# Performance work log

Hardware: AMD Instinct MI355X
Metric: run time of the kernel (lower is better)

Reference implementation:

```python
import jax, jax.numpy as jnp
import numpy as np

BN_EPS = 1e-5

def _batchnorm(z, gamma, beta):
    # training-mode BN over node axis, biased variance (matches torch normalization)
    mean = jnp.mean(z, axis=0)
    var = jnp.mean((z - mean) ** 2, axis=0)
    return (z - mean) * jax.lax.rsqrt(var + BN_EPS) * gamma + beta

def setup_inputs() -> dict:
    key = jax.random.key(0)
    N, E, D, L = 100000, 1000000, 128, 2
    ks = jax.random.split(key, 8)
    x = jax.random.normal(ks[0], (N, D), dtype=jnp.float32)
    edge_index = jax.random.randint(ks[1], (2, E), 0, N, dtype=jnp.int64)
    s = 1.0 / np.sqrt(D)
    W1 = jax.random.uniform(ks[2], (L, D, D), jnp.float32, -s, s)
    b1 = jax.random.uniform(ks[3], (L, D), jnp.float32, -s, s)
    W2 = jax.random.uniform(ks[4], (L, D, D), jnp.float32, -s, s)
    b2 = jax.random.uniform(ks[5], (L, D), jnp.float32, -s, s)
    g1 = jnp.ones((L, D), jnp.float32); bt1 = jnp.zeros((L, D), jnp.float32)
    g_out = jnp.ones((L, D), jnp.float32); bt_out = jnp.zeros((L, D), jnp.float32)
    eps = jnp.zeros((L,), jnp.float32)  # GIN eps, init 0
    return {"x": x, "edge_index": edge_index, "W1": W1, "b1": b1, "g1": g1,
            "bt1": bt1, "W2": W2, "b2": b2, "eps": eps, "g_out": g_out, "bt_out": bt_out}

def reference(x, edge_index, W1, b1, g1, bt1, W2, b2, eps, g_out, bt_out):
    N = x.shape[0]
    L = W1.shape[0]
    src, dst = edge_index[0], edge_index[1]
    h = x
    for l in range(L):
        # message: relu(x_j) gathered along edges; aggregate: scatter-add to dst
        msg = jax.nn.relu(h[src])                                  # [E, D]
        aggr = jax.ops.segment_sum(msg, dst, num_segments=N)       # [N, D]
        z = (1.0 + eps[l]) * h + aggr
        # GINConv MLP: Linear -> BN -> ReLU -> Linear
        z = z @ W1[l].T + b1[l]
        z = jax.nn.relu(_batchnorm(z, g1[l], bt1[l]))
        z = z @ W2[l].T + b2[l]
        # outer per-layer BatchNorm
        z = _batchnorm(z, g_out[l], bt_out[l])
        if l < L - 1:
            z = jax.nn.relu(z)
        # dropout is identity in eval mode
        h = z
    return h
```

## Files before the change

### kernel.cpp

```cpp
#include <hip/hip_runtime.h>
#include <hip/hip_fp16.h>

typedef unsigned int u32;
typedef unsigned short u16;
typedef __attribute__((ext_vector_type(8))) _Float16 f16x8;
typedef __attribute__((ext_vector_type(4))) float f32x4;

#define DF 128
#define NBUCK 256
#define BUCK_SHIFT 9
#define BUCK_SIZE 512
#define P2_CHUNK 4096
#define NCOPY 16
#define STATW (NCOPY * DF)
#define CS16 136

__device__ __forceinline__ __half2 u2h2(u32 x) { union { u32 u; __half2 h; } v; v.u = x; return v.h; }
__device__ __forceinline__ u32 h22u(__half2 h) { union { u32 u; __half2 h; } v; v.h = h; return v.u; }
__device__ __forceinline__ u32 pack2h(float a, float b) { return h22u(__floats2half2_rn(a, b)); }

__device__ __forceinline__ u32 pkmax_u(u32 a, u32 b) {
  u32 r;
  asm("v_pk_max_f16 %0, %1, %2" : "=v"(r) : "v"(a), "v"(b));
  return r;
}
__device__ __forceinline__ __half2 hmax2(__half2 a, __half2 b) {
  return u2h2(pkmax_u(h22u(a), h22u(b)));
}

__global__ void k_cvt_f32_f16(const float* __restrict__ in, u16* __restrict__ out, int n4) {
  int i = blockIdx.x * blockDim.x + threadIdx.x;
  if (i >= n4) return;
  float4 v = ((const float4*)in)[i];
  ((uint2*)out)[i] = make_uint2(pack2h(v.x, v.y), pack2h(v.z, v.w));
}

__global__ __launch_bounds__(256) void k_p1(const int* __restrict__ dst,
                                            int* __restrict__ bucketCount, int E) {
  __shared__ int h[NBUCK];
  int t = threadIdx.x;
  h[t] = 0;
  __syncthreads();
  for (int e = blockIdx.x * 256 + t; e < E; e += gridDim.x * 256)
    atomicAdd(&h[((u32)dst[e]) >> BUCK_SHIFT], 1);
  __syncthreads();
  if (h[t]) atomicAdd(&bucketCount[t], h[t]);
}

__global__ __launch_bounds__(256) void k_pscan(const int* __restrict__ bucketCount,
                                               int* __restrict__ bucketStart,
                                               int* __restrict__ bucketCursor,
                                               int* __restrict__ rowptr, int N, int E) {
  __shared__ int sh[NBUCK];
  int t = threadIdx.x;
  int c = bucketCount[t];
  sh[t] = c;
  __syncthreads();
  for (int o = 1; o < 256; o <<= 1) {
    int v = (t >= o) ? sh[t - o] : 0;
    __syncthreads();
    sh[t] += v;
    __syncthreads();
  }
  int excl = sh[t] - c;
  bucketStart[t] = excl;
  bucketCursor[t] = excl;
  if (t == 255) { bucketStart[256] = sh[255]; rowptr[N] = E; }
}

__global__ __launch_bounds__(256) void k_p2(const int* __restrict__ src,
                                            const int* __restrict__ dst,
                                            int* __restrict__ bucketCursor,
                                            uint2* __restrict__ part, int E) {
  __shared__ int h[NBUCK], hs[NBUCK], base[NBUCK];
  __shared__ int total;
  __shared__ uint2 buf[P2_CHUNK];
  int t = threadIdx.x;
  int e0 = blockIdx.x * P2_CHUNK;
  h[t] = 0;
  __syncthreads();
  int myb[16], myr[16];
  uint2 mye[16];
  #pragma unroll
  for (int k = 0; k < 16; k++) {
    int e = e0 + k * 256 + t;
    myb[k] = -1;
    if (e < E) {
      int s = src[e], d = dst[e];
      mye[k] = make_uint2((u32)s, (u32)d);
      myb[k] = ((u32)d) >> BUCK_SHIFT;
      myr[k] = atomicAdd(&h[myb[k]], 1);
    }
  }
  __syncthreads();
  int hc = h[t];
  hs[t] = hc;
  __syncthreads();
  for (int o = 1; o < 256; o <<= 1) {
    int v = (t >= o) ? hs[t - o] : 0;
    __syncthreads();
    hs[t] += v;
    __syncthreads();
  }
  if (t == 255) total = hs[255];
  int excl = hs[t] - hc;
  base[t] = hc ? atomicAdd(&bucketCursor[t], hc) : 0;
  __syncthreads();
  hs[t] = excl;
  __syncthreads();
  #pragma unroll
  for (int k = 0; k < 16; k++)
    if (myb[k] >= 0) buf[hs[myb[k]] + myr[k]] = mye[k];
  __syncthreads();
  int tot = total;
  for (int i = t; i < tot; i += 256) {
    uint2 ed = buf[i];
    int b = ed.y >> BUCK_SHIFT;
    part[base[b] + (i - hs[b])] = ed;
  }
}

__global__ __launch_bounds__(256) void k_p3(const uint2* __restrict__ part,
                                            const int* __restrict__ bucketStart,
                                            int* __restrict__ rowptr,
                                            int* __restrict__ adj, int N) {
  __shared__ int deg[BUCK_SIZE], cur[BUCK_SIZE], psum[256];
  int b = blockIdx.x, t = threadIdx.x;
  int nodeBase = b << BUCK_SHIFT;
  int eb = bucketStart[b], ee = bucketStart[b + 1];
  deg[t] = 0; deg[t + 256] = 0;
  __syncthreads();
  for (int e = eb + t; e < ee; e += 256)
    atomicAdd(&deg[(int)part[e].y - nodeBase], 1);
  __syncthreads();
  int a0 = deg[2 * t], a1 = deg[2 * t + 1];
  psum[t] = a0 + a1;
  __syncthreads();
  for (int o = 1; o < 256; o <<= 1) {
    int v = (t >= o) ? psum[t - o] : 0;
    __syncthreads();
    psum[t] += v;
    __syncthreads();
  }
  int basep = psum[t] - (a0 + a1);
  int p0 = eb + basep, p1 = eb + basep + a0;
  cur[2 * t] = p0; cur[2 * t + 1] = p1;
  int n0 = nodeBase + 2 * t, n1 = nodeBase + 2 * t + 1;
  if (n0 < N) rowptr[n0] = p0;
  if (n1 < N) rowptr[n1] = p1;
  __syncthreads();
  for (int e = eb + t; e < ee; e += 256) {
    uint2 ed = part[e];
    int pos = atomicAdd(&cur[(int)ed.y - nodeBase], 1);
    adj[pos] = (int)ed.x;
  }
}

__global__ void k_aggr(const u16* __restrict__ hin,
                       const int* __restrict__ rowptr, const int* __restrict__ adj,
                       const float* __restrict__ epsArr, int layer,
                       const float* __restrict__ aAff, const float* __restrict__ cAff,
                       int selfRelu,
                       u16* __restrict__ z, int N) {
  int wid = (blockIdx.x * blockDim.x + threadIdx.x) >> 6;
  if (wid >= N) return;
  int lane = threadIdx.x & 63;
  int g = lane >> 4, f = lane & 15;
  const uint4* h4 = (const uint4*)hin;
  float e1 = 1.0f + epsArr[layer];
  __half2 zero2 = __floats2half2_rn(0.0f, 0.0f);

  float av[8], cv[8];
  if (aAff) {
    float4 a0 = *(const float4*)(aAff + f * 8);
    float4 a1 = *(const float4*)(aAff + f * 8 + 4);
    float4 c0 = *(const float4*)(cAff + f * 8);
    float4 c1 = *(const float4*)(cAff + f * 8 + 4);
    av[0] = a0.x; av[1] = a0.y; av[2] = a0.z; av[3] = a0.w;
    av[4] = a1.x; av[5] = a1.y; av[6] = a1.z; av[7] = a1.w;
    cv[0] = c0.x; cv[1] = c0.y; cv[2] = c0.z; cv[3] = c0.w;
    cv[4] = c1.x; cv[5] = c1.y; cv[6] = c1.z; cv[7] = c1.w;
  } else {
    #pragma unroll
    for (int k = 0; k < 8; k++) { av[k] = 1.0f; cv[k] = 0.0f; }
  }
  __half2 a2[4], c2[4], cm2[4], acc2[4];
  #pragma unroll
  for (int k = 0; k < 4; k++) {
    a2[k] = __floats2half2_rn(av[2 * k], av[2 * k + 1]);
    c2[k] = __floats2half2_rn(cv[2 * k], cv[2 * k + 1]);
    cm2[k] = hmax2(c2[k], zero2);
    acc2[k] = zero2;
  }

  int b = rowptr[wid], e = rowptr[wid + 1];
  int inv = 0;
  for (int p = b; p < e; p += 16) {
    int i0 = p + g, i1 = p + 4 + g, i2 = p + 8 + g, i3 = p + 12 + g;
    uint4 v0 = make_uint4(0, 0, 0, 0), v1 = make_uint4(0, 0, 0, 0);
    uint4 v2 = make_uint4(0, 0, 0, 0), v3 = make_uint4(0, 0, 0, 0);
    if (i0 < e) v0 = h4[(size_t)(u32)adj[i0] * 16 + f]; else inv++;
    if (i1 < e) v1 = h4[(size_t)(u32)adj[i1] * 16 + f]; else inv++;
    if (i2 < e) v2 = h4[(size_t)(u32)adj[i2] * 16 + f]; else inv++;
    if (i3 < e) v3 = h4[(size_t)(u32)adj[i3] * 16 + f]; else inv++;
    u32 w0[4] = {v0.x, v0.y, v0.z, v0.w};
    u32 w1[4] = {v1.x, v1.y, v1.z, v1.w};
    u32 w2[4] = {v2.x, v2.y, v2.z, v2.w};
    u32 w3[4] = {v3.x, v3.y, v3.z, v3.w};
    #pragma unroll
    for (int k = 0; k < 4; k++) {
      acc2[k] = __hadd2(acc2[k], hmax2(__hfma2(a2[k], u2h2(w0[k]), c2[k]), zero2));
      acc2[k] = __hadd2(acc2[k], hmax2(__hfma2(a2[k], u2h2(w1[k]), c2[k]), zero2));
      acc2[k] = __hadd2(acc2[k], hmax2(__hfma2(a2[k], u2h2(w2[k]), c2[k]), zero2));
      acc2[k] = __hadd2(acc2[k], hmax2(__hfma2(a2[k], u2h2(w3[k]), c2[k]), zero2));
    }
  }
  __half2 inv2 = __floats2half2_rn((float)inv, (float)inv);
  #pragma unroll
  for (int k = 0; k < 4; k++) {
    acc2[k] = __hsub2(acc2[k], __hmul2(inv2, cm2[k]));
    acc2[k] = __hadd2(acc2[k], u2h2(__shfl_xor(h22u(acc2[k]), 16)));
    acc2[k] = __hadd2(acc2[k], u2h2(__shfl_xor(h22u(acc2[k]), 32)));
  }

  if (g == 0) {
    uint4 sv = h4[(size_t)wid * 16 + f];
    u32 sw[4] = {sv.x, sv.y, sv.z, sv.w};
    u32 o[4];
    #pragma unroll
    for (int k = 0; k < 4; k++) {
      float2 s = __half22float2(u2h2(sw[k]));
      float lo = fmaf(av[2 * k], s.x, cv[2 * k]);
      float hi = fmaf(av[2 * k + 1], s.y, cv[2 * k + 1]);
      if (selfRelu) { lo = fmaxf(lo, 0.0f); hi = fmaxf(hi, 0.0f); }
      float2 nb = __half22float2(acc2[k]);
      o[k] = pack2h(fmaf(e1, lo, nb.x), fmaf(e1, hi, nb.y));
    }
    ((uint4*)z)[(size_t)wid * 16 + f] = make_uint4(o[0], o[1], o[2], o[3]);
  }
}

__global__ __launch_bounds__(256, 4) void k_gemm(
    const u16* __restrict__ A, const u16* __restrict__ W, const float* __restrict__ bias,
    const float* __restrict__ Sprev, const float* __restrict__ Qprev,
    const float* __restrict__ gprev, const float* __restrict__ btprev, int trans,
    float* __restrict__ statS, float* __restrict__ statQ,
    u16* __restrict__ out, int Nrows) {
  __shared__ __align__(16) char smem[128 * CS16 * 2 + 512];
  u16* lA = (u16*)smem;
  u16* sC = (u16*)smem;
  __half2* sA2 = (__half2*)(smem + 128 * CS16 * 2);
  __half2* sC2 = (__half2*)(smem + 128 * CS16 * 2 + 256);
  int tid = threadIdx.x;
  int rowBase = blockIdx.x * 128;

  if (trans) {
    if (tid < 64) {
      float aa[2], cc[2];
      #pragma unroll
      for (int j = 0; j < 2; j++) {
        int col = tid * 2 + j;
        float Sv = 0.f, Qv = 0.f;
        #pragma unroll
        for (int i = 0; i < NCOPY; i++) { Sv += Sprev[i * DF + col]; Qv += Qprev[i * DF + col]; }
        float inv_n = 1.0f / (float)Nrows;
        float mean = Sv * inv_n;
        float var = fmaxf(Qv * inv_n - mean * mean, 0.0f);
        float iv = rsqrtf(var + 1e-5f);
        float a = gprev[col] * iv;
        aa[j] = a;
        cc[j] = btprev[col] - mean * a;
      }
      sA2[tid] = __floats2half2_rn(aa[0], aa[1]);
      sC2[tid] = __floats2half2_rn(cc[0], cc[1]);
    }
    __syncthreads();
  }

  #pragma unroll
  for (int cc = 0; cc < 8; cc++) {
    int c = tid + cc * 256;
    int lane = c & 63, rt = (c >> 6) & 7, kt = c >> 9;
    int m = lane & 15, quad = lane >> 4;
    int grow = rowBase + rt * 16 + m;
    int gk = kt * 32 + quad * 8;
    uint4 val = make_uint4(0, 0, 0, 0);
    if (grow < Nrows) val = *(const uint4*)(A + (size_t)grow * DF + gk);
    if (trans) {
      uint4 aw = ((const uint4*)sA2)[gk >> 3];
      uint4 cw = ((const uint4*)sC2)[gk >> 3];
      val.x = pkmax_u(h22u(__hfma2(u2h2(aw.x), u2h2(val.x), u2h2(cw.x))), 0u);
      val.y = pkmax_u(h22u(__hfma2(u2h2(aw.y), u2h2(val.y), u2h2(cw.y))), 0u);
      val.z = pkmax_u(h22u(__hfma2(u2h2(aw.z), u2h2(val.z), u2h2(cw.z))), 0u);
      val.w = pkmax_u(h22u(__hfma2(u2h2(aw.w), u2h2(val.w), u2h2(cw.w))), 0u);
    }
    ((uint4*)lA)[c] = val;
  }
  __syncthreads();

  int lane = tid & 63, w = tid >> 6;
  int rq = w >> 1, cq = w & 1;
  int mcol = lane & 15, quad = lane >> 4;
  f32x4 acc[4][4];
  #pragma unroll
  for (int i = 0; i < 4; i++)
    #pragma unroll
    for (int j = 0; j < 4; j++) acc[i][j] = (f32x4){0.f, 0.f, 0.f, 0.f};

  const f16x8* pA = (const f16x8*)lA;
  #pragma unroll
  for (int kt = 0; kt < 4; kt++) {
    f16x8 af[4], bfr[4];
    #pragma unroll
    for (int i = 0; i < 4; i++) af[i] = pA[(kt * 8 + rq * 4 + i) * 64 + lane];
    #pragma unroll
    for (int j = 0; j < 4; j++)
      bfr[j] = *(const f16x8*)(W + ((cq * 4 + j) * 16 + mcol) * DF + kt * 32 + quad * 8);
    #pragma unroll
    for (int i = 0; i < 4; i++)
      #pragma unroll
      for (int j = 0; j < 4; j++)
        acc[i][j] = __builtin_amdgcn_mfma_f32_16x16x32_f16(af[i], bfr[j], acc[i][j], 0, 0, 0);
  }

  __syncthreads();

  float colS[4] = {0, 0, 0, 0}, colQ[4] = {0, 0, 0, 0};
  #pragma unroll
  for (int j = 0; j < 4; j++) {
    int col = (cq * 4 + j) * 16 + mcol;
    float bv = bias[col];
    #pragma unroll
    for (int i = 0; i < 4; i++) {
      int rel0 = (rq * 4 + i) * 16 + quad * 4;
      #pragma unroll
      for (int r = 0; r < 4; r++) {
        int rel = rel0 + r;
        float v = acc[i][j][r] + bv;
        sC[rel * CS16 + col] = (u16)h22u(__floats2half2_rn(v, 0.0f));
        if (rowBase + rel < Nrows) { colS[j] += v; colQ[j] += v * v; }
      }
    }
  }
  __syncthreads();

  #pragma unroll
  for (int k = 0; k < 8; k++) {
    int idx = k * 256 + tid;
    int rel = idx >> 4;
    int c0 = (idx & 15) * 8;
    int row = rowBase + rel;
    if (row < Nrows) {
      uint4 o = *(const uint4*)(sC + rel * CS16 + c0);
      *(uint4*)(out + (size_t)row * DF + c0) = o;
    }
  }

  int copyOff = (blockIdx.x & (NCOPY - 1)) * DF;
  #pragma unroll
  for (int j = 0; j < 4; j++) {
    float s = colS[j], q = colQ[j];
    s += __shfl_xor(s, 16); q += __shfl_xor(q, 16);
    s += __shfl_xor(s, 32); q += __shfl_xor(q, 32);
    if (quad == 0) {
      int col = (cq * 4 + j) * 16 + mcol;
      atomicAdd(&statS[copyOff + col], s);
      atomicAdd(&statQ[copyOff + col], q);
    }
  }
}

__global__ void k_finalize(const float* __restrict__ s, const float* __restrict__ q,
                           const float* __restrict__ gamma, const float* __restrict__ beta,
                           float* __restrict__ a, float* __restrict__ c, int Nrows) {
  int t = threadIdx.x;
  if (t < DF) {
    float S = 0.f, Q = 0.f;
    #pragma unroll
    for (int i = 0; i < NCOPY; i++) { S += s[i * DF + t]; Q += q[i * DF + t]; }
    float inv_n = 1.0f / (float)Nrows;
    float mean = S * inv_n;
    float var = fmaxf(Q * inv_n - mean * mean, 0.0f);
    float iv = rsqrtf(var + 1e-5f);
    float av = gamma[t] * iv;
    a[t] = av;
    c[t] = beta[t] - mean * av;
  }
}

__global__ __launch_bounds__(256) void k_bnout_f32(
    const u16* __restrict__ u, const float* __restrict__ S, const float* __restrict__ Q,
    const float* __restrict__ gamma, const float* __restrict__ beta, int Nrows,
    float* __restrict__ out, int n8) {
  __shared__ float sAf[DF], sCf[DF];
  int tid = threadIdx.x;
  if (tid < DF) {
    float Sv = 0.f, Qv = 0.f;
    #pragma unroll
    for (int i = 0; i < NCOPY; i++) { Sv += S[i * DF + tid]; Qv += Q[i * DF + tid]; }
    float inv_n = 1.0f / (float)Nrows;
    float mean = Sv * inv_n;
    float var = fmaxf(Qv * inv_n - mean * mean, 0.0f);
    float iv = rsqrtf(var + 1e-5f);
    float a = gamma[tid] * iv;
    sAf[tid] = a;
    sCf[tid] = beta[tid] - mean * a;
  }
  __syncthreads();
  for (int i = blockIdx.x * 256 + tid; i < n8; i += gridDim.x * 256) {
    int col = (i * 8) & 127;
    float4 a0 = *(const float4*)(sAf + col), a1v = *(const float4*)(sAf + col + 4);
    float4 c0 = *(const float4*)(sCf + col), c1v = *(const float4*)(sCf + col + 4);
    uint4 v = ((const uint4*)u)[i];
    float2 f0 = __half22float2(u2h2(v.x));
    float2 f1 = __half22float2(u2h2(v.y));
    float2 f2 = __half22float2(u2h2(v.z));
    float2 f3 = __half22float2(u2h2(v.w));
    float4 o0, o1;
    o0.x = fmaf(a0.x, f0.x, c0.x);
    o0.y = fmaf(a0.y, f0.y, c0.y);
    o0.z = fmaf(a0.z, f1.x, c0.z);
    o0.w = fmaf(a0.w, f1.y, c0.w);
    o1.x = fmaf(a1v.x, f2.x, c1v.x);
    o1.y = fmaf(a1v.y, f2.y, c1v.y);
    o1.z = fmaf(a1v.z, f3.x, c1v.z);
    o1.w = fmaf(a1v.w, f3.y, c1v.w);
    ((float4*)out)[i * 2] = o0;
    ((float4*)out)[i * 2 + 1] = o1;
  }
}

extern "C" void kernel_launch(void* const* d_in, const int* in_sizes, int n_in,
                              void* d_out, int out_size, void* d_ws, size_t ws_size,
                              hipStream_t stream) {
  const float* x    = (const float*)d_in[0];
  const int*   ei   = (const int*)d_in[1];
  const float* W1   = (const float*)d_in[2];
  const float* b1   = (const float*)d_in[3];
  const float* g1   = (const float*)d_in[4];
  const float* bt1  = (const float*)d_in[5];
  const float* W2   = (const float*)d_in[6];
  const float* b2   = (const float*)d_in[7];
  const float* eps  = (const float*)d_in[8];
  const float* gout = (const float*)d_in[9];
  const float* btout= (const float*)d_in[10];

  int N = in_sizes[0] / DF;
  int E = in_sizes[1] / 2;
  int L = in_sizes[8];

  char* ws = (char*)d_ws;
  size_t off = 0;
  auto alloc = [&](size_t bytes) -> void* {
    void* p = ws + off;
    off += (bytes + 255) & ~(size_t)255;
    return p;
  };
  u16* Xb     = (u16*)alloc((size_t)N * DF * 2);
  u16* bufA   = (u16*)alloc((size_t)N * DF * 2);
  u16* bufB   = (u16*)alloc((size_t)N * DF * 2);
  int* rowptr = (int*)alloc((size_t)(N + 1) * 4);
  int* adj    = (int*)alloc((size_t)E * 4);
  uint2* part = (uint2*)alloc((size_t)E * 8);
  int* bCount = (int*)alloc(NBUCK * 4);
  int* bStart = (int*)alloc((NBUCK + 1) * 4);
  int* bCur   = (int*)alloc(NBUCK * 4);
  u16* W1b    = (u16*)alloc((size_t)L * DF * DF * 2);
  u16* W2b    = (u16*)alloc((size_t)L * DF * DF * 2);
  float* stats= (float*)alloc((size_t)L * 4 * STATW * 4);
  float* coefs= (float*)alloc((size_t)L * 4 * DF * 4);

  hipMemsetAsync(bCount, 0, NBUCK * 4, stream);
  hipMemsetAsync(stats, 0, (size_t)L * 4 * STATW * 4, stream);

  int n4x = N * DF / 4;
  k_cvt_f32_f16<<<(n4x + 255) / 256, 256, 0, stream>>>(x, Xb, n4x);
  int n4w = L * DF * DF / 4;
  k_cvt_f32_f16<<<(n4w + 255) / 256, 256, 0, stream>>>(W1, W1b, n4w);
  k_cvt_f32_f16<<<(n4w + 255) / 256, 256, 0, stream>>>(W2, W2b, n4w);

  const int* srcI = ei;
  const int* dstI = ei + E;
  int nbuckets = (N + BUCK_SIZE - 1) >> BUCK_SHIFT;
  k_p1<<<512, 256, 0, stream>>>(dstI, bCount, E);
  k_pscan<<<1, 256, 0, stream>>>(bCount, bStart, bCur, rowptr, N, E);
  k_p2<<<(E + P2_CHUNK - 1) / P2_CHUNK, 256, 0, stream>>>(srcI, dstI, bCur, part, E);
  k_p3<<<nbuckets, 256, 0, stream>>>(part, bStart, rowptr, adj, N);

  int gblocks = (N + 127) / 128;
  int n8 = N * DF / 8;
  const u16* Hcur = Xb;
  const float* aPrev = nullptr;
  const float* cPrev = nullptr;
  int selfRelu = 0;
  for (int l = 0; l < L; l++) {
    float* S1 = stats + (size_t)(l * 4 + 0) * STATW;
    float* Q1 = stats + (size_t)(l * 4 + 1) * STATW;
    float* S2 = stats + (size_t)(l * 4 + 2) * STATW;
    float* Q2 = stats + (size_t)(l * 4 + 3) * STATW;
    float* a2 = coefs + (size_t)(l * 4 + 2) * DF;
    float* c2 = coefs + (size_t)(l * 4 + 3) * DF;
    u16* z = (l & 1) ? bufB : bufA;
    u16* t = (l & 1) ? bufA : bufB;
    u16* u = z;

    k_aggr<<<(N + 3) / 4, 256, 0, stream>>>(Hcur, rowptr, adj, eps, l,
                                            aPrev, cPrev, selfRelu, z, N);
    k_gemm<<<gblocks, 256, 0, stream>>>(z, W1b + l * DF * DF, b1 + l * DF,
                                        nullptr, nullptr, nullptr, nullptr, 0,
                                        S1, Q1, t, N);
    k_gemm<<<gblocks, 256, 0, stream>>>(t, W2b + l * DF * DF, b2 + l * DF,
                                        S1, Q1, g1 + l * DF, bt1 + l * DF, 1,
                                        S2, Q2, u, N);
    if (l < L - 1) {
      k_finalize<<<1, 128, 0, stream>>>(S2, Q2, gout + l * DF, btout + l * DF, a2, c2, N);
      aPrev = a2; cPrev = c2; selfRelu = 1;
      Hcur = u;
    } else {
      k_bnout_f32<<<2048, 256, 0, stream>>>(u, S2, Q2, gout + l * DF, btout + l * DF,
                                            N, (float*)d_out, n8);
    }
  }
}
```

Measured before the change: 371.0 us.

## Fuse neighbor aggregation into first GEMM, staging aggregated tile in LDS

Merges the gather/scatter aggregation kernel with the first linear layer. Each 256-thread block aggregates 128 nodes, with each wave handling two nodes at a time, writes the fp16 results straight into the MFMA A-fragment layout in shared memory, then runs the GEMM and accumulates the BN statistics. This removes the global write and re-read of the aggregated z buffer and one launch per layer. In exchange, parallelism in the memory-bound gather drops from one node per wave to 32 nodes per wave processed serially, which can hurt latency hiding.

New measurement: 395.4 us. +6.6%, slower.

```diff
diff --git a/kernel.cpp b/kernel.cpp
--- a/kernel.cpp
+++ b/kernel.cpp
@@ -156,19 +156,24 @@
   }
 }
 
-__global__ void k_aggr(const u16* __restrict__ hin,
-                       const int* __restrict__ rowptr, const int* __restrict__ adj,
-                       const float* __restrict__ epsArr, int layer,
-                       const float* __restrict__ aAff, const float* __restrict__ cAff,
-                       int selfRelu,
-                       u16* __restrict__ z, int N) {
-  int wid = (blockIdx.x * blockDim.x + threadIdx.x) >> 6;
-  if (wid >= N) return;
-  int lane = threadIdx.x & 63;
+__global__ __launch_bounds__(256, 4) void k_ag(
+    const u16* __restrict__ hin, const int* __restrict__ rowptr,
+    const int* __restrict__ adj, const float* __restrict__ epsArr, int layer,
+    const float* __restrict__ aAff, const float* __restrict__ cAff, int selfRelu,
+    const u16* __restrict__ W, const float* __restrict__ bias,
+    float* __restrict__ statS, float* __restrict__ statQ,
+    u16* __restrict__ out, int N) {
+  __shared__ __align__(16) char smem[128 * CS16 * 2];
+  u16* lA = (u16*)smem;
+  u16* sC = (u16*)smem;
+  int tid = threadIdx.x;
+  int lane = tid & 63, w = tid >> 6;
   int g = lane >> 4, f = lane & 15;
+  int rowBase = blockIdx.x * 128;
   const uint4* h4 = (const uint4*)hin;
   float e1 = 1.0f + epsArr[layer];
   __half2 zero2 = __floats2half2_rn(0.0f, 0.0f);
+  uint4 z4 = make_uint4(0, 0, 0, 0);
 
   float av[8], cv[8];
   if (aAff) {
@@ -184,59 +189,165 @@
     #pragma unroll
     for (int k = 0; k < 8; k++) { av[k] = 1.0f; cv[k] = 0.0f; }
   }
-  __half2 a2[4], c2[4], cm2[4], acc2[4];
+  __half2 a2[4], c2[4], cm2[4];
   #pragma unroll
   for (int k = 0; k < 4; k++) {
     a2[k] = __floats2half2_rn(av[2 * k], av[2 * k + 1]);
     c2[k] = __floats2half2_rn(cv[2 * k], cv[2 * k + 1]);
     cm2[k] = hmax2(c2[k], zero2);
-    acc2[k] = zero2;
-  }
-
-  int b = rowptr[wid], e = rowptr[wid + 1];
-  int inv = 0;
-  for (int p = b; p < e; p += 16) {
-    int i0 = p + g, i1 = p + 4 + g, i2 = p + 8 + g, i3 = p + 12 + g;
-    uint4 v0 = make_uint4(0, 0, 0, 0), v1 = make_uint4(0, 0, 0, 0);
-    uint4 v2 = make_uint4(0, 0, 0, 0), v3 = make_uint4(0, 0, 0, 0);
-    if (i0 < e) v0 = h4[(size_t)(u32)adj[i0] * 16 + f]; else inv++;
-    if (i1 < e) v1 = h4[(size_t)(u32)adj[i1] * 16 + f]; else inv++;
-    if (i2 < e) v2 = h4[(size_t)(u32)adj[i2] * 16 + f]; else inv++;
-    if (i3 < e) v3 = h4[(size_t)(u32)adj[i3] * 16 + f]; else inv++;
-    u32 w0[4] = {v0.x, v0.y, v0.z, v0.w};
-    u32 w1[4] = {v1.x, v1.y, v1.z, v1.w};
-    u32 w2[4] = {v2.x, v2.y, v2.z, v2.w};
-    u32 w3[4] = {v3.x, v3.y, v3.z, v3.w};
+  }
+
+  for (int s = 0; s < 32; s += 2) {
+    int relA = w * 32 + s, relB = relA + 1;
+    int nA = rowBase + relA, nB = rowBase + relB;
+    __half2 accA[4], accB[4];
+    #pragma unroll
+    for (int k = 0; k < 4; k++) { accA[k] = zero2; accB[k] = zero2; }
+    int invA = 0, invB = 0;
+    int bAi = 0, eAi = 0, bBi = 0, eBi = 0;
+    if (nA < N) { bAi = rowptr[nA]; eAi = rowptr[nA + 1]; }
+    if (nB < N) { bBi = rowptr[nB]; eBi = rowptr[nB + 1]; }
+    int pA = bAi, pB = bBi;
+    while (pA < eAi || pB < eBi) {
+      uint4 va0 = z4, va1 = z4, va2 = z4, va3 = z4;
+      uint4 vb0 = z4, vb1 = z4, vb2 = z4, vb3 = z4;
+      if (pA + g      < eAi) va0 = h4[(size_t)(u32)adj[pA + g]      * 16 + f]; else invA++;
+      if (pA + 4 + g  < eAi) va1 = h4[(size_t)(u32)adj[pA + 4 + g]  * 16 + f]; else invA++;
+      if (pA + 8 + g  < eAi) va2 = h4[(size_t)(u32)adj[pA + 8 + g]  * 16 + f]; else invA++;
+      if (pA + 12 + g < eAi) va3 = h4[(size_t)(u32)adj[pA + 12 + g] * 16 + f]; else invA++;
+      if (pB + g      < eBi) vb0 = h4[(size_t)(u32)adj[pB + g]      * 16 + f]; else invB++;
+      if (pB + 4 + g  < eBi) vb1 = h4[(size_t)(u32)adj[pB + 4 + g]  * 16 + f]; else invB++;
+      if (pB + 8 + g  < eBi) vb2 = h4[(size_t)(u32)adj[pB + 8 + g]  * 16 + f]; else invB++;
+      if (pB + 12 + g < eBi) vb3 = h4[(size_t)(u32)adj[pB + 12 + g] * 16 + f]; else invB++;
+      u32 wa[4][4] = {{va0.x, va0.y, va0.z, va0.w}, {va1.x, va1.y, va1.z, va1.w},
+                      {va2.x, va2.y, va2.z, va2.w}, {va3.x, va3.y, va3.z, va3.w}};
+      u32 wb[4][4] = {{vb0.x, vb0.y, vb0.z, vb0.w}, {vb1.x, vb1.y, vb1.z, vb1.w},
+                      {vb2.x, vb2.y, vb2.z, vb2.w}, {vb3.x, vb3.y, vb3.z, vb3.w}};
+      #pragma unroll
+      for (int q = 0; q < 4; q++) {
+        #pragma unroll
+        for (int k = 0; k < 4; k++) {
+          accA[k] = __hadd2(accA[k], hmax2(__hfma2(a2[k], u2h2(wa[q][k]), c2[k]), zero2));
+          accB[k] = __hadd2(accB[k], hmax2(__hfma2(a2[k], u2h2(wb[q][k]), c2[k]), zero2));
+        }
+      }
+      pA += 16; pB += 16;
+    }
+    __half2 iA2 = __floats2half2_rn((float)invA, (float)invA);
+    __half2 iB2 = __floats2half2_rn((float)invB, (float)invB);
     #pragma unroll
     for (int k = 0; k < 4; k++) {
-      acc2[k] = __hadd2(acc2[k], hmax2(__hfma2(a2[k], u2h2(w0[k]), c2[k]), zero2));
-      acc2[k] = __hadd2(acc2[k], hmax2(__hfma2(a2[k], u2h2(w1[k]), c2[k]), zero2));
-      acc2[k] = __hadd2(acc2[k], hmax2(__hfma2(a2[k], u2h2(w2[k]), c2[k]), zero2));
-      acc2[k] = __hadd2(acc2[k], hmax2(__hfma2(a2[k], u2h2(w3[k]), c2[k]), zero2));
-    }
-  }
-  __half2 inv2 = __floats2half2_rn((float)inv, (float)inv);
-  #pragma unroll
-  for (int k = 0; k < 4; k++) {
-    acc2[k] = __hsub2(acc2[k], __hmul2(inv2, cm2[k]));
-    acc2[k] = __hadd2(acc2[k], u2h2(__shfl_xor(h22u(acc2[k]), 16)));
-    acc2[k] = __hadd2(acc2[k], u2h2(__shfl_xor(h22u(acc2[k]), 32)));
-  }
-
-  if (g == 0) {
-    uint4 sv = h4[(size_t)wid * 16 + f];
-    u32 sw[4] = {sv.x, sv.y, sv.z, sv.w};
-    u32 o[4];
-    #pragma unroll
-    for (int k = 0; k < 4; k++) {
-      float2 s = __half22float2(u2h2(sw[k]));
-      float lo = fmaf(av[2 * k], s.x, cv[2 * k]);
-      float hi = fmaf(av[2 * k + 1], s.y, cv[2 * k + 1]);
-      if (selfRelu) { lo = fmaxf(lo, 0.0f); hi = fmaxf(hi, 0.0f); }
-      float2 nb = __half22float2(acc2[k]);
-      o[k] = pack2h(fmaf(e1, lo, nb.x), fmaf(e1, hi, nb.y));
-    }
-    ((uint4*)z)[(size_t)wid * 16 + f] = make_uint4(o[0], o[1], o[2], o[3]);
+      accA[k] = __hsub2(accA[k], __hmul2(iA2, cm2[k]));
+      accB[k] = __hsub2(accB[k], __hmul2(iB2, cm2[k]));
+      accA[k] = __hadd2(accA[k], u2h2(__shfl_xor(h22u(accA[k]), 16)));
+      accA[k] = __hadd2(accA[k], u2h2(__shfl_xor(h22u(accA[k]), 32)));
+      accB[k] = __hadd2(accB[k], u2h2(__shfl_xor(h22u(accB[k]), 16)));
+      accB[k] = __hadd2(accB[k], u2h2(__shfl_xor(h22u(accB[k]), 32)));
+    }
+    if (g == 0) {
+      int cA = (f >> 2) * 512 + (relA >> 4) * 64 + (f & 3) * 16 + (relA & 15);
+      int cB = (f >> 2) * 512 + (relB >> 4) * 64 + (f & 3) * 16 + (relB & 15);
+      uint4 oA = z4, oB = z4;
+      if (nA < N) {
+        uint4 sv = h4[(size_t)nA * 16 + f];
+        u32 sw[4] = {sv.x, sv.y, sv.z, sv.w};
+        #pragma unroll
+        for (int k = 0; k < 4; k++) {
+          float2 sf = __half22float2(u2h2(sw[k]));
+          float lo = fmaf(av[2 * k], sf.x, cv[2 * k]);
+          float hi = fmaf(av[2 * k + 1], sf.y, cv[2 * k + 1]);
+          if (selfRelu) { lo = fmaxf(lo, 0.0f); hi = fmaxf(hi, 0.0f); }
+          float2 nb = __half22float2(accA[k]);
+          ((u32*)&oA)[k] = pack2h(fmaf(e1, lo, nb.x), fmaf(e1, hi, nb.y));
+        }
+      }
+      if (nB < N) {
+        uint4 sv = h4[(size_t)nB * 16 + f];
+        u32 sw[4] = {sv.x, sv.y, sv.z, sv.w};
+        #pragma unroll
+        for (int k = 0; k < 4; k++) {
+          float2 sf = __half22float2(u2h2(sw[k]));
+          float lo = fmaf(av[2 * k], sf.x, cv[2 * k]);
+          float hi = fmaf(av[2 * k + 1], sf.y, cv[2 * k + 1]);
+          if (selfRelu) { lo = fmaxf(lo, 0.0f); hi = fmaxf(hi, 0.0f); }
+          float2 nb = __half22float2(accB[k]);
+          ((u32*)&oB)[k] = pack2h(fmaf(e1, lo, nb.x), fmaf(e1, hi, nb.y));
+        }
+      }
+      ((uint4*)lA)[cA] = oA;
+      ((uint4*)lA)[cB] = oB;
+    }
+  }
+  __syncthreads();
+
+  int rq = w >> 1, cq = w & 1;
+  int mcol = lane & 15, quad = lane >> 4;
+  f32x4 acc[4][4];
+  #pragma unroll
+  for (int i = 0; i < 4; i++)
+    #pragma unroll
+    for (int j = 0; j < 4; j++) acc[i][j] = (f32x4){0.f, 0.f, 0.f, 0.f};
+
+  const f16x8* pLA = (const f16x8*)lA;
+  #pragma unroll
+  for (int kt = 0; kt < 4; kt++) {
+    f16x8 af[4], bfr[4];
+    #pragma unroll
+    for (int i = 0; i < 4; i++) af[i] = pLA[(kt * 8 + rq * 4 + i) * 64 + lane];
+    #pragma unroll
+    for (int j = 0; j < 4; j++)
+      bfr[j] = *(const f16x8*)(W + ((cq * 4 + j) * 16 + mcol) * DF + kt * 32 + quad * 8);
+    #pragma unroll
+    for (int i = 0; i < 4; i++)
+      #pragma unroll
+      for (int j = 0; j < 4; j++)
+        acc[i][j] = __builtin_amdgcn_mfma_f32_16x16x32_f16(af[i], bfr[j], acc[i][j], 0, 0, 0);
+  }
+
+  __syncthreads();
+
+  float colS[4] = {0, 0, 0, 0}, colQ[4] = {0, 0, 0, 0};
+  #pragma unroll
+  for (int j = 0; j < 4; j++) {
+    int col = (cq * 4 + j) * 16 + mcol;
+    float bv = bias[col];
+    #pragma unroll
+    for (int i = 0; i < 4; i++) {
+      int rel0 = (rq * 4 + i) * 16 + quad * 4;
+      #pragma unroll
+      for (int r = 0; r < 4; r++) {
+        int rel = rel0 + r;
+        float v = acc[i][j][r] + bv;
+        sC[rel * CS16 + col] = (u16)h22u(__floats2half2_rn(v, 0.0f));
+        if (rowBase + rel < N) { colS[j] += v; colQ[j] += v * v; }
+      }
+    }
+  }
+  __syncthreads();
+
+  #pragma unroll
+  for (int k = 0; k < 8; k++) {
+    int idx = k * 256 + tid;
+    int rel = idx >> 4;
+    int c0 = (idx & 15) * 8;
+    int row = rowBase + rel;
+    if (row < N) {
+      uint4 o = *(const uint4*)(sC + rel * CS16 + c0);
+      *(uint4*)(out + (size_t)row * DF + c0) = o;
+    }
+  }
+
+  int copyOff = (blockIdx.x & (NCOPY - 1)) * DF;
+  #pragma unroll
+  for (int j = 0; j < 4; j++) {
+    float s = colS[j], q = colQ[j];
+    s += __shfl_xor(s, 16); q += __shfl_xor(q, 16);
+    s += __shfl_xor(s, 32); q += __shfl_xor(q, 32);
+    if (quad == 0) {
+      int col = (cq * 4 + j) * 16 + mcol;
+      atomicAdd(&statS[copyOff + col], s);
+      atomicAdd(&statQ[copyOff + col], q);
+    }
   }
 }
 
@@ -307,12 +418,12 @@
     #pragma unroll
     for (int j = 0; j < 4; j++) acc[i][j] = (f32x4){0.f, 0.f, 0.f, 0.f};
 
-  const f16x8* pA = (const f16x8*)lA;
+  const f16x8* pLA = (const f16x8*)lA;
   #pragma unroll
   for (int kt = 0; kt < 4; kt++) {
     f16x8 af[4], bfr[4];
     #pragma unroll
-    for (int i = 0; i < 4; i++) af[i] = pA[(kt * 8 + rq * 4 + i) * 64 + lane];
+    for (int i = 0; i < 4; i++) af[i] = pLA[(kt * 8 + rq * 4 + i) * 64 + lane];
     #pragma unroll
     for (int j = 0; j < 4; j++)
       bfr[j] = *(const f16x8*)(W + ((cq * 4 + j) * 16 + mcol) * DF + kt * 32 + quad * 8);
@@ -500,15 +611,13 @@
     float* Q2 = stats + (size_t)(l * 4 + 3) * STATW;
     float* a2 = coefs + (size_t)(l * 4 + 2) * DF;
     float* c2 = coefs + (size_t)(l * 4 + 3) * DF;
-    u16* z = (l & 1) ? bufB : bufA;
-    u16* t = (l & 1) ? bufA : bufB;
-    u16* u = z;
-
-    k_aggr<<<(N + 3) / 4, 256, 0, stream>>>(Hcur, rowptr, adj, eps, l,
-                                            aPrev, cPrev, selfRelu, z, N);
-    k_gemm<<<gblocks, 256, 0, stream>>>(z, W1b + l * DF * DF, b1 + l * DF,
-                                        nullptr, nullptr, nullptr, nullptr, 0,
-                                        S1, Q1, t, N);
+    u16* t = bufB;
+    u16* u = bufA;
+
+    k_ag<<<gblocks, 256, 0, stream>>>(Hcur, rowptr, adj, eps, l,
+                                      aPrev, cPrev, selfRelu,
+                                      W1b + l * DF * DF, b1 + l * DF,
+                                      S1, Q1, t, N);
     k_gemm<<<gblocks, 256, 0, stream>>>(t, W2b + l * DF * DF, b2 + l * DF,
                                         S1, Q1, g1 + l * DF, bt1 + l * DF, 1,
                                         S2, Q2, u, N);
```
